# Kernel tuning notes

Measured on AMD Instinct MI355X. Metric: run time of the kernel, lower is better.

## Reference

```python
import jax, jax.numpy as jnp
import numpy as np

LN_EPS = 1e-6  # flax.linen.LayerNorm default


def setup_inputs() -> dict:
    key = jax.random.key(0)
    ks = jax.random.split(key, 16)
    N_TOT, M = 32768, 12            # total atoms, neighbors per atom
    ORIG, EDGE = 92, 41             # CGCNN atom / edge feature dims
    F, H, L = 128, 256, 3           # atom_fea_len, h_fea_len, n_conv

    def w(k, shape, fan_in):
        return jax.random.normal(k, shape, dtype=jnp.float32) / np.sqrt(fan_in).astype(np.float32)

    return {
        "atom_fea": jax.random.normal(ks[0], (N_TOT, ORIG), dtype=jnp.float32),
        "nbr_fea": jax.random.normal(ks[1], (N_TOT, M, EDGE), dtype=jnp.float32),
        "nbr_fea_idx": jax.random.randint(ks[2], (N_TOT, M), 0, N_TOT),
        # embedding Dense
        "W_embed": w(ks[3], (ORIG, F), ORIG), "b_embed": jnp.zeros((F,), jnp.float32),
        # per-conv-layer stacked params [L, ...]
        "W_center": w(ks[4], (L, F, F), F), "b_center": jnp.zeros((L, F), jnp.float32),
        "W_nbr": w(ks[5], (L, F, F), F), "b_nbr": jnp.zeros((L, F), jnp.float32),
        "W_edge": w(ks[6], (L, EDGE, F), EDGE), "b_edge": jnp.zeros((L, F), jnp.float32),
        "W_gate": w(ks[7], (L, F, F), F), "b_gate": jnp.zeros((L, F), jnp.float32),
        "W_mag": w(ks[8], (L, F, F), F), "b_mag": jnp.zeros((L, F), jnp.float32),
        "ln_scale": jnp.ones((L, F), jnp.float32), "ln_bias": jnp.zeros((L, F), jnp.float32),
        # readout: Dense(h) -> softplus -> Dense(1)
        "W_h": w(ks[9], (F, H), F), "b_h": jnp.zeros((H,), jnp.float32),
        "W_out": w(ks[10], (H, 1), H), "b_out": jnp.zeros((1,), jnp.float32),
        "batch_size": 128,
        "n_atoms_per_crystal": 256,
    }


def _layernorm(x, scale, bias):
    mu = jnp.mean(x, axis=-1, keepdims=True)
    var = jnp.mean(jnp.square(x - mu), axis=-1, keepdims=True)
    return (x - mu) * jax.lax.rsqrt(var + LN_EPS) * scale + bias


def reference(atom_fea, nbr_fea, nbr_fea_idx, W_embed, b_embed,
              W_center, b_center, W_nbr, b_nbr, W_edge, b_edge,
              W_gate, b_gate, W_mag, b_mag, ln_scale, ln_bias,
              W_h, b_h, W_out, b_out, batch_size, n_atoms_per_crystal):
    n_conv = W_center.shape[0]
    x = atom_fea @ W_embed + b_embed                       # [N, F]
    for i in range(n_conv):
        atom_nbr = jnp.take(x, nbr_fea_idx, axis=0)        # [N, M, F] gather
        # Dense on tiled center == Dense on center then broadcast
        phi_c = (x @ W_center[i] + b_center[i])[:, None, :]   # [N, 1, F]
        phi_n = atom_nbr @ W_nbr[i] + b_nbr[i]                # [N, M, F]
        phi_e = nbr_fea @ W_edge[i] + b_edge[i]               # [N, M, F]
        inter = phi_c * phi_n * phi_e                          # [N, M, F]
        gate = jax.nn.sigmoid(inter @ W_gate[i] + b_gate[i])
        mag = jax.nn.softplus(inter @ W_mag[i] + b_mag[i])
        nbr_sumed = jnp.sum(gate * mag, axis=1)               # [N, F]
        x = x + _layernorm(nbr_sumed, ln_scale[i], ln_bias[i])
    E_site = jax.nn.softplus(x @ W_h + b_h) @ W_out + b_out   # [N, 1]
    return jnp.sum(E_site.reshape(batch_size, n_atoms_per_crystal), axis=1, keepdims=True)  # [B, 1]
```

## Files before the change

kernel.cpp:

```cpp
#include <hip/hip_runtime.h>
#include <math.h>

#define N_TOT 32768
#define M_NBR 12
#define ORIG  92
#define EDGE  41
#define FD    128
#define HD    256
#define APC   256
#define NCRY  128
#define NROW  (N_TOT * M_NBR)
#define EST   48

#define WF_PER_LAYER 73728
#define WF_EMBED     12288
#define WF_H         32768

#define ISW(row, col) ((((row) << 7) + (col)) ^ (((row) & 7) << 3))

typedef __attribute__((ext_vector_type(8))) short bf16x8;
typedef __attribute__((ext_vector_type(4))) float f32x4;

union BF8 { bf16x8 v; unsigned u[4]; };

__device__ __forceinline__ unsigned pk2(float lo, float hi) {
    unsigned r;
    asm("v_cvt_pk_bf16_f32 %0, %1, %2" : "=v"(r) : "v"(lo), "v"(hi));
    return r;
}
__device__ __forceinline__ short f2bf(float f) { return (short)pk2(f, f); }
__device__ __forceinline__ float bf2f(short s) {
    union { unsigned u; float f; } v; v.u = ((unsigned)(unsigned short)s) << 16;
    return v.f;
}
__device__ __forceinline__ float softplus_f(float x) {
    return fmaxf(x, 0.0f) + 0.6931471805599453f * __log2f(1.0f + __expf(-fabsf(x)));
}
__device__ __forceinline__ float sigmoid_f(float x) {
    return __builtin_amdgcn_rcpf(1.0f + __expf(-x));
}

__global__ __launch_bounds__(256) void swizzle_kernel(
    const float* __restrict__ Wc_all, const float* __restrict__ Wn_all,
    const float* __restrict__ We_all, const float* __restrict__ Wg_all,
    const float* __restrict__ Wm_all, const float* __restrict__ W_embed,
    const float* __restrict__ W_h, const float* __restrict__ be_all,
    short* __restrict__ dst_all)
{
    int gid = blockIdx.x * 256 + threadIdx.x;
    if (gid >= 33280) return;
    const float* W; short* dst; int K_real, fid, stride, l, nt, kt;
    const float* brow = nullptr;
    if (gid < 27648) {
        int layer = gid / 9216;
        int rem = gid - layer * 9216;
        short* dbase = dst_all + layer * WF_PER_LAYER;
        if (rem < 2048)      { W = Wc_all + layer * 16384; dst = dbase;         K_real = 128; fid = rem; }
        else if (rem < 4096) { W = Wn_all + layer * 16384; dst = dbase + 16384; K_real = 128; fid = rem - 2048; }
        else if (rem < 5120) { W = We_all + layer * 5248;  dst = dbase + 32768; K_real = 41;  fid = rem - 4096;
                               brow = be_all + layer * FD; }
        else if (rem < 7168) { W = Wg_all + layer * 16384; dst = dbase + 40960; K_real = 128; fid = rem - 5120; }
        else                 { W = Wm_all + layer * 16384; dst = dbase + 57344; K_real = 128; fid = rem - 7168; }
        stride = 128; l = fid & 63; nt = (fid >> 6) & 7; kt = fid >> 9;
    } else if (gid < 29184) {
        fid = gid - 27648;
        W = W_embed; dst = dst_all + 3 * WF_PER_LAYER; K_real = ORIG; stride = 128;
        l = fid & 63; nt = (fid >> 6) & 7; kt = fid >> 9;
    } else {
        fid = gid - 29184;
        W = W_h; dst = dst_all + 3 * WF_PER_LAYER + WF_EMBED; K_real = 128; stride = 256;
        l = fid & 63; nt = (fid >> 6) & 15; kt = fid >> 10;
    }
    int n = nt * 16 + (l & 15), kb = kt * 32 + (l >> 4) * 8;
    bf16x8 v;
    #pragma unroll
    for (int j = 0; j < 8; ++j) {
        int k = kb + j;
        short val;
        if (k < K_real)                    val = f2bf(W[k * stride + n]);
        else if (brow != nullptr && k == 41) val = f2bf(brow[n]);
        else                               val = 0;
        v[j] = val;
    }
    *(bf16x8*)(dst + fid * 8) = v;
}

__global__ __launch_bounds__(256) void prep_ebf_kernel(
    const float* __restrict__ nbr_fea, short* __restrict__ ebf)
{
    const int r = blockIdx.x * 256 + threadIdx.x;
    const float* ep = nbr_fea + (long)r * EDGE;
    unsigned u[24];
    #pragma unroll
    for (int j = 0; j < 20; ++j) u[j] = pk2(ep[2 * j], ep[2 * j + 1]);
    u[20] = pk2(ep[40], 1.0f);
    u[21] = 0u; u[22] = 0u; u[23] = 0u;
    uint4* dst = (uint4*)(ebf + (long)r * EST);
    #pragma unroll
    for (int j = 0; j < 6; ++j)
        dst[j] = make_uint4(u[4 * j], u[4 * j + 1], u[4 * j + 2], u[4 * j + 3]);
}

__global__ __launch_bounds__(256) void embed_mfma_kernel(
    const float* __restrict__ atom_fea, const short* __restrict__ wef,
    const float* __restrict__ b, float* __restrict__ x, short* __restrict__ xbf)
{
    const int tid = threadIdx.x;
    const int w = tid >> 6, lane = tid & 63;
    const int q = lane >> 4, m = lane & 15;
    const int a0 = blockIdx.x * 64;
    const int arow = a0 + w * 16 + m;

    BF8 aA[3];
    const float* ap = atom_fea + (long)arow * ORIG;
    #pragma unroll
    for (int kt = 0; kt < 3; ++kt) {
        const int kb = kt * 32 + q * 8;
        BF8 t;
        if (kb + 7 < ORIG) {
            const float4 u0 = *(const float4*)(ap + kb);
            const float4 u1 = *(const float4*)(ap + kb + 4);
            t.u[0] = pk2(u0.x, u0.y); t.u[1] = pk2(u0.z, u0.w);
            t.u[2] = pk2(u1.x, u1.y); t.u[3] = pk2(u1.z, u1.w);
        } else {
            const float4 u0 = *(const float4*)(ap + kb);
            t.u[0] = pk2(u0.x, u0.y); t.u[1] = pk2(u0.z, u0.w);
            t.u[2] = 0u; t.u[3] = 0u;
        }
        aA[kt] = t;
    }

    #pragma unroll
    for (int ct = 0; ct < 8; ++ct) {
        f32x4 C = {0.f, 0.f, 0.f, 0.f};
        #pragma unroll
        for (int kt = 0; kt < 3; ++kt)
            C = __builtin_amdgcn_mfma_f32_16x16x32_bf16(
                    *(const bf16x8*)(wef + ((kt * 8 + ct) * 64 + lane) * 8), aA[kt].v, C, 0, 0, 0);
        const float4 bv = *(const float4*)(b + ct * 16 + q * 4);
        const float o0 = C[0] + bv.x, o1 = C[1] + bv.y, o2 = C[2] + bv.z, o3 = C[3] + bv.w;
        const long base = ((long)arow << 7) + ct * 16 + q * 4;
        *(float4*)(x + base) = make_float4(o0, o1, o2, o3);
        *(uint2*)(xbf + base) = make_uint2(pk2(o0, o1), pk2(o2, o3));
    }
}

__global__ __launch_bounds__(256) void pcy_kernel(
    const short* __restrict__ xbf, const short* __restrict__ wcf,
    const short* __restrict__ wnf, const float* __restrict__ bc,
    const float* __restrict__ bn, float* __restrict__ phic_g,
    float* __restrict__ y_g)
{
    const int tid = threadIdx.x;
    const int w = tid >> 6, lane = tid & 63;
    const int q = lane >> 4, m = lane & 15;
    const int arow = blockIdx.x * 64 + w * 16 + m;

    bf16x8 aX[4];
    #pragma unroll
    for (int kt = 0; kt < 4; ++kt)
        aX[kt] = *(const bf16x8*)(xbf + ((long)arow << 7) + kt * 32 + q * 8);

    #pragma unroll
    for (int ct = 0; ct < 8; ++ct) {
        f32x4 Cc = {0.f, 0.f, 0.f, 0.f};
        f32x4 Cn = {0.f, 0.f, 0.f, 0.f};
        #pragma unroll
        for (int kt = 0; kt < 4; ++kt) {
            const int fo = ((kt * 8 + ct) * 64 + lane) * 8;
            Cc = __builtin_amdgcn_mfma_f32_16x16x32_bf16(*(const bf16x8*)(wcf + fo), aX[kt], Cc, 0, 0, 0);
            Cn = __builtin_amdgcn_mfma_f32_16x16x32_bf16(*(const bf16x8*)(wnf + fo), aX[kt], Cn, 0, 0, 0);
        }
        const float4 bcv = *(const float4*)(bc + ct * 16 + q * 4);
        const float4 bnv = *(const float4*)(bn + ct * 16 + q * 4);
        const long base = ((long)arow << 7) + ct * 16 + q * 4;
        *(float4*)(phic_g + base) = make_float4(Cc[0] + bcv.x, Cc[1] + bcv.y, Cc[2] + bcv.z, Cc[3] + bcv.w);
        *(float4*)(y_g + base)    = make_float4(Cn[0] + bnv.x, Cn[1] + bnv.y, Cn[2] + bnv.z, Cn[3] + bnv.w);
    }
}

__global__ __launch_bounds__(256) void conv_mfma_kernel(
    const float* __restrict__ x_in,
    float* __restrict__ x_out, short* __restrict__ xbf_out,
    const float* __restrict__ phic_g, const float* __restrict__ y_g,
    const short* __restrict__ ebf, const int* __restrict__ nbr_idx,
    const short* __restrict__ wf,
    const float* __restrict__ bg, const float* __restrict__ bm,
    const float* __restrict__ lns, const float* __restrict__ lnb,
    const short* __restrict__ wc_next, const short* __restrict__ wn_next,
    const float* __restrict__ bc_next, const float* __restrict__ bn_next,
    float* __restrict__ phic_out, float* __restrict__ y_out)
{
    __shared__ short inter_s[192 * 128];

    const int tid = threadIdx.x;
    const int w = tid >> 6, lane = tid & 63;
    const int q = lane >> 4, m = lane & 15;
    const int a0 = blockIdx.x * 16;
    const long r0 = (long)a0 * M_NBR;

    const short* We = wf + 32768;
    const short* Wg = wf + 40960;
    const short* Wm = wf + 57344;

    int rl[3], idxv[3], atomg[3];
    #pragma unroll
    for (int i = 0; i < 3; ++i) {
        rl[i] = (w * 3 + i) * 16 + m;
        idxv[i] = nbr_idx[r0 + rl[i]];
        atomg[i] = a0 + rl[i] / 12;
    }

    bf16x8 aE[3][2];
    #pragma unroll
    for (int i = 0; i < 3; ++i) {
        const short* ep = ebf + (r0 + rl[i]) * EST;
        aE[i][0] = *(const bf16x8*)(ep + q * 8);
        if (q < 2) {
            aE[i][1] = *(const bf16x8*)(ep + 32 + q * 8);
        } else {
            BF8 z; z.u[0] = 0u; z.u[1] = 0u; z.u[2] = 0u; z.u[3] = 0u;
            aE[i][1] = z.v;
        }
    }

    #pragma unroll
    for (int ct = 0; ct < 8; ++ct) {
        f32x4 Ce[3];
        #pragma unroll
        for (int i = 0; i < 3; ++i) Ce[i] = (f32x4){0.f, 0.f, 0.f, 0.f};
        #pragma unroll
        for (int kt = 0; kt < 2; ++kt) {
            const bf16x8 efr = *(const bf16x8*)(We + ((kt * 8 + ct) * 64 + lane) * 8);
            #pragma unroll
            for (int i = 0; i < 3; ++i)
                Ce[i] = __builtin_amdgcn_mfma_f32_16x16x32_bf16(efr, aE[i][kt], Ce[i], 0, 0, 0);
        }
        #pragma unroll
        for (int i = 0; i < 3; ++i)
            *(uint2*)(inter_s + ISW(rl[i], ct * 16 + q * 4)) =
                make_uint2(pk2(Ce[i][0], Ce[i][1]), pk2(Ce[i][2], Ce[i][3]));
    }

    bf16x8 aI[3][4];
    #pragma unroll
    for (int i = 0; i < 3; ++i) {
        const float* pp = phic_g + ((long)atomg[i] << 7);
        const float* yp = y_g + ((long)idxv[i] << 7);
        #pragma unroll
        for (int kt = 0; kt < 4; ++kt) {
            const int k0 = kt * 32 + q * 8;
            const float4 pa = *(const float4*)(pp + k0);
            const float4 pb = *(const float4*)(pp + k0 + 4);
            const float4 ya = *(const float4*)(yp + k0);
            const float4 yb = *(const float4*)(yp + k0 + 4);
            const bf16x8 ef = *(const bf16x8*)(inter_s + ISW(rl[i], k0));
            const float v0 = pa.x * ya.x * bf2f(ef[0]);
            const float v1 = pa.y * ya.y * bf2f(ef[1]);
            const float v2 = pa.z * ya.z * bf2f(ef[2]);
            const float v3 = pa.w * ya.w * bf2f(ef[3]);
            const float v4 = pb.x * yb.x * bf2f(ef[4]);
            const float v5 = pb.y * yb.y * bf2f(ef[5]);
            const float v6 = pb.z * yb.z * bf2f(ef[6]);
            const float v7 = pb.w * yb.w * bf2f(ef[7]);
            BF8 t;
            t.u[0] = pk2(v0, v1); t.u[1] = pk2(v2, v3);
            t.u[2] = pk2(v4, v5); t.u[3] = pk2(v6, v7);
            aI[i][kt] = t.v;
        }
    }

    #pragma unroll
    for (int ct = 0; ct < 8; ++ct) {
        f32x4 Cg[3], Cm[3];
        #pragma unroll
        for (int i = 0; i < 3; ++i) {
            Cg[i] = (f32x4){0.f, 0.f, 0.f, 0.f};
            Cm[i] = (f32x4){0.f, 0.f, 0.f, 0.f};
        }
        #pragma unroll
        for (int kt = 0; kt < 4; ++kt) {
            const bf16x8 gfr = *(const bf16x8*)(Wg + ((kt * 8 + ct) * 64 + lane) * 8);
            const bf16x8 mfr = *(const bf16x8*)(Wm + ((kt * 8 + ct) * 64 + lane) * 8);
            #pragma unroll
            for (int i = 0; i < 3; ++i) {
                Cg[i] = __builtin_amdgcn_mfma_f32_16x16x32_bf16(gfr, aI[i][kt], Cg[i], 0, 0, 0);
                Cm[i] = __builtin_amdgcn_mfma_f32_16x16x32_bf16(mfr, aI[i][kt], Cm[i], 0, 0, 0);
            }
        }
        const float4 bgv = *(const float4*)(bg + ct * 16 + q * 4);
        const float4 bmv = *(const float4*)(bm + ct * 16 + q * 4);
        #pragma unroll
        for (int i = 0; i < 3; ++i) {
            const float v0 = sigmoid_f(Cg[i][0] + bgv.x) * softplus_f(Cm[i][0] + bmv.x);
            const float v1 = sigmoid_f(Cg[i][1] + bgv.y) * softplus_f(Cm[i][1] + bmv.y);
            const float v2 = sigmoid_f(Cg[i][2] + bgv.z) * softplus_f(Cm[i][2] + bmv.z);
            const float v3 = sigmoid_f(Cg[i][3] + bgv.w) * softplus_f(Cm[i][3] + bmv.w);
            *(uint2*)(inter_s + ISW(rl[i], ct * 16 + q * 4)) =
                make_uint2(pk2(v0, v1), pk2(v2, v3));
        }
    }

    BF8 ob;
    {
        const int a = tid >> 4;
        const int cg = tid & 15;
        float s8[8];
        #pragma unroll
        for (int j = 0; j < 8; ++j) s8[j] = 0.f;
        #pragma unroll
        for (int nb = 0; nb < 12; ++nb) {
            const bf16x8 p = *(const bf16x8*)(inter_s + ISW(a * 12 + nb, cg * 8));
            #pragma unroll
            for (int j = 0; j < 8; ++j) s8[j] += bf2f(p[j]);
        }
        float lsum = 0.f, lsq = 0.f;
        #pragma unroll
        for (int j = 0; j < 8; ++j) { lsum += s8[j]; lsq += s8[j] * s8[j]; }
        #pragma unroll
        for (int off = 1; off < 16; off <<= 1) {
            lsum += __shfl_xor(lsum, off, 64);
            lsq  += __shfl_xor(lsq,  off, 64);
        }
        const float mu = lsum * (1.0f / FD);
        float var = lsq * (1.0f / FD) - mu * mu;
        var = fmaxf(var, 0.0f);
        const float inv = rsqrtf(var + 1e-6f);
        const long xb = ((long)(a0 + a) << 7) + cg * 8;
        float xv[8], sc[4], sc2[4], bb[4], bb2[4];
        *(float4*)&xv[0] = *(const float4*)(x_in + xb);
        *(float4*)&xv[4] = *(const float4*)(x_in + xb + 4);
        *(float4*)&sc[0]  = *(const float4*)(lns + cg * 8);
        *(float4*)&sc2[0] = *(const float4*)(lns + cg * 8 + 4);
        *(float4*)&bb[0]  = *(const float4*)(lnb + cg * 8);
        *(float4*)&bb2[0] = *(const float4*)(lnb + cg * 8 + 4);
        float o[8];
        #pragma unroll
        for (int j = 0; j < 4; ++j) {
            o[j]     = xv[j]     + (s8[j]     - mu) * inv * sc[j]  + bb[j];
            o[j + 4] = xv[j + 4] + (s8[j + 4] - mu) * inv * sc2[j] + bb2[j];
        }
        ob.u[0] = pk2(o[0], o[1]); ob.u[1] = pk2(o[2], o[3]);
        ob.u[2] = pk2(o[4], o[5]); ob.u[3] = pk2(o[6], o[7]);
        *(float4*)(x_out + xb)     = make_float4(o[0], o[1], o[2], o[3]);
        *(float4*)(x_out + xb + 4) = make_float4(o[4], o[5], o[6], o[7]);
        *(bf16x8*)(xbf_out + xb)   = ob.v;
    }

    if (wc_next) {
        __syncthreads();
        *(bf16x8*)(inter_s + ISW(tid >> 4, (tid & 15) * 8)) = ob.v;
        __syncthreads();
        bf16x8 aX[4];
        #pragma unroll
        for (int kt = 0; kt < 4; ++kt)
            aX[kt] = *(const bf16x8*)(inter_s + ISW(m, kt * 32 + q * 8));
        #pragma unroll
        for (int ii = 0; ii < 2; ++ii) {
            const int ct = w * 2 + ii;
            f32x4 Cc = {0.f, 0.f, 0.f, 0.f};
            f32x4 Cn2 = {0.f, 0.f, 0.f, 0.f};
            #pragma unroll
            for (int kt = 0; kt < 4; ++kt) {
                const int fo = ((kt * 8 + ct) * 64 + lane) * 8;
                Cc  = __builtin_amdgcn_mfma_f32_16x16x32_bf16(*(const bf16x8*)(wc_next + fo), aX[kt], Cc, 0, 0, 0);
                Cn2 = __builtin_amdgcn_mfma_f32_16x16x32_bf16(*(const bf16x8*)(wn_next + fo), aX[kt], Cn2, 0, 0, 0);
            }
            const float4 bcv = *(const float4*)(bc_next + ct * 16 + q * 4);
            const float4 bnv = *(const float4*)(bn_next + ct * 16 + q * 4);
            const long base = ((long)(a0 + m) << 7) + ct * 16 + q * 4;
            *(float4*)(phic_out + base) =
                make_float4(Cc[0] + bcv.x, Cc[1] + bcv.y, Cc[2] + bcv.z, Cc[3] + bcv.w);
            *(float4*)(y_out + base) =
                make_float4(Cn2[0] + bnv.x, Cn2[1] + bnv.y, Cn2[2] + bnv.z, Cn2[3] + bnv.w);
        }
    }
}

__global__ __launch_bounds__(256) void readout_mfma_kernel(
    const short* __restrict__ xbf, const short* __restrict__ whf,
    const float* __restrict__ bh, const float* __restrict__ Wo,
    const float* __restrict__ bo, float* __restrict__ out)
{
    const int tid = threadIdx.x;
    const int w = tid >> 6, lane = tid & 63;
    const int q = lane >> 4, m = lane & 15;
    const int a0 = blockIdx.x * 64;
    const int arow = a0 + w * 16 + m;

    bf16x8 aX[4];
    #pragma unroll
    for (int kt = 0; kt < 4; ++kt)
        aX[kt] = *(const bf16x8*)(xbf + ((long)arow << 7) + kt * 32 + q * 8);

    float e[4] = {0.f, 0.f, 0.f, 0.f};
    #pragma unroll
    for (int nt = 0; nt < 16; ++nt) {
        f32x4 C = {0.f, 0.f, 0.f, 0.f};
        #pragma unroll
        for (int kt = 0; kt < 4; ++kt)
            C = __builtin_amdgcn_mfma_f32_16x16x32_bf16(
                    aX[kt], *(const bf16x8*)(whf + ((kt * 16 + nt) * 64 + lane) * 8), C, 0, 0, 0);
        const int col = nt * 16 + m;
        const float bhv = bh[col], wov = Wo[col];
        #pragma unroll
        for (int r = 0; r < 4; ++r)
            e[r] += softplus_f(C[r] + bhv) * wov;
    }
    float esum = e[0] + e[1] + e[2] + e[3];
    #pragma unroll
    for (int off = 32; off > 0; off >>= 1)
        esum += __shfl_xor(esum, off, 64);
    if (lane == 0)
        atomicAdd(&out[a0 / APC], esum + 16.0f * bo[0]);
}

__global__ void zero_out_kernel(float* __restrict__ out) {
    if (threadIdx.x < NCRY) out[threadIdx.x] = 0.0f;
}

extern "C" void kernel_launch(void* const* d_in, const int* in_sizes, int n_in,
                              void* d_out, int out_size, void* d_ws, size_t ws_size,
                              hipStream_t stream) {
    const float* atom_fea = (const float*)d_in[0];
    const float* nbr_fea  = (const float*)d_in[1];
    const int*   nbr_idx  = (const int*)d_in[2];
    const float* W_embed  = (const float*)d_in[3];
    const float* b_embed  = (const float*)d_in[4];
    const float* W_center = (const float*)d_in[5];
    const float* b_center = (const float*)d_in[6];
    const float* W_nbr    = (const float*)d_in[7];
    const float* b_nbr    = (const float*)d_in[8];
    const float* W_edge   = (const float*)d_in[9];
    const float* b_edge   = (const float*)d_in[10];
    const float* W_gate   = (const float*)d_in[11];
    const float* b_gate   = (const float*)d_in[12];
    const float* W_mag    = (const float*)d_in[13];
    const float* b_mag    = (const float*)d_in[14];
    const float* ln_scale = (const float*)d_in[15];
    const float* ln_bias  = (const float*)d_in[16];
    const float* W_h      = (const float*)d_in[17];
    const float* b_h      = (const float*)d_in[18];
    const float* W_out    = (const float*)d_in[19];
    const float* b_out    = (const float*)d_in[20];

    float* out = (float*)d_out;
    const size_t NX = (size_t)N_TOT * FD;
    float* xA    = (float*)d_ws;
    float* xB    = xA + NX;
    float* phic  = xB + NX;
    float* yA    = phic + NX;
    float* yB    = yA + NX;
    short* xbfA  = (short*)(yB + NX);
    short* xbfB  = xbfA + NX;
    short* ebf   = xbfB + NX;
    short* wfrag = ebf + (size_t)NROW * EST;

    swizzle_kernel<<<130, 256, 0, stream>>>(W_center, W_nbr, W_edge, W_gate, W_mag,
                                            W_embed, W_h, b_edge, wfrag);
    prep_ebf_kernel<<<NROW / 256, 256, 0, stream>>>(nbr_fea, ebf);
    embed_mfma_kernel<<<N_TOT / 64, 256, 0, stream>>>(
        atom_fea, wfrag + 3 * WF_PER_LAYER, b_embed, xA, xbfA);
    pcy_kernel<<<N_TOT / 64, 256, 0, stream>>>(
        xbfA, wfrag, wfrag + 16384, b_center, b_nbr, phic, yA);

    conv_mfma_kernel<<<N_TOT / 16, 256, 0, stream>>>(
        xA, xB, xbfB, phic, yA, ebf, nbr_idx, wfrag,
        b_gate, b_mag, ln_scale, ln_bias,
        wfrag + WF_PER_LAYER, wfrag + WF_PER_LAYER + 16384,
        b_center + FD, b_nbr + FD, phic, yB);
    conv_mfma_kernel<<<N_TOT / 16, 256, 0, stream>>>(
        xB, xA, xbfA, phic, yB, ebf, nbr_idx, wfrag + WF_PER_LAYER,
        b_gate + FD, b_mag + FD, ln_scale + FD, ln_bias + FD,
        wfrag + 2 * WF_PER_LAYER, wfrag + 2 * WF_PER_LAYER + 16384,
        b_center + 2 * FD, b_nbr + 2 * FD, phic, yA);
    conv_mfma_kernel<<<N_TOT / 16, 256, 0, stream>>>(
        xA, xB, xbfB, phic, yA, ebf, nbr_idx, wfrag + 2 * WF_PER_LAYER,
        b_gate + 2 * FD, b_mag + 2 * FD, ln_scale + 2 * FD, ln_bias + 2 * FD,
        nullptr, nullptr, nullptr, nullptr, nullptr, nullptr);

    zero_out_kernel<<<1, 128, 0, stream>>>(out);
    readout_mfma_kernel<<<N_TOT / 64, 256, 0, stream>>>(
        xbfB, wfrag + 3 * WF_PER_LAYER + WF_EMBED, b_h, W_out, b_out, out);
}
```

Measured before the change: 436.2 us.

## Fuse edge prep, embedding and first-layer projections into one front kernel

```diff
diff --git a/kernel.cpp b/kernel.cpp
--- a/kernel.cpp
+++ b/kernel.cpp
@@ -11,6 +11,8 @@
 #define NCRY  128
 #define NROW  (N_TOT * M_NBR)
 #define EST   48
+#define NBLK_EMBED (N_TOT / 64)
+#define NBLK_PREP  (NROW / 256)
 
 #define WF_PER_LAYER 73728
 #define WF_EMBED     12288
@@ -77,39 +79,46 @@
     for (int j = 0; j < 8; ++j) {
         int k = kb + j;
         short val;
-        if (k < K_real)                    val = f2bf(W[k * stride + n]);
+        if (k < K_real)                      val = f2bf(W[k * stride + n]);
         else if (brow != nullptr && k == 41) val = f2bf(brow[n]);
-        else                               val = 0;
+        else                                 val = 0;
         v[j] = val;
     }
     *(bf16x8*)(dst + fid * 8) = v;
 }
 
-__global__ __launch_bounds__(256) void prep_ebf_kernel(
+__global__ __launch_bounds__(256) void front_kernel(
+    const float* __restrict__ atom_fea, const short* __restrict__ wef,
+    const float* __restrict__ b, float* __restrict__ x, short* __restrict__ xbf,
+    const short* __restrict__ wcf, const short* __restrict__ wnf,
+    const float* __restrict__ bc, const float* __restrict__ bn,
+    float* __restrict__ phic_g, float* __restrict__ y_g,
     const float* __restrict__ nbr_fea, short* __restrict__ ebf)
 {
-    const int r = blockIdx.x * 256 + threadIdx.x;
-    const float* ep = nbr_fea + (long)r * EDGE;
-    unsigned u[24];
-    #pragma unroll
-    for (int j = 0; j < 20; ++j) u[j] = pk2(ep[2 * j], ep[2 * j + 1]);
-    u[20] = pk2(ep[40], 1.0f);
-    u[21] = 0u; u[22] = 0u; u[23] = 0u;
-    uint4* dst = (uint4*)(ebf + (long)r * EST);
-    #pragma unroll
-    for (int j = 0; j < 6; ++j)
-        dst[j] = make_uint4(u[4 * j], u[4 * j + 1], u[4 * j + 2], u[4 * j + 3]);
-}
-
-__global__ __launch_bounds__(256) void embed_mfma_kernel(
-    const float* __restrict__ atom_fea, const short* __restrict__ wef,
-    const float* __restrict__ b, float* __restrict__ x, short* __restrict__ xbf)
-{
+    __shared__ short xs_s[4 * 16 * 128];
+
     const int tid = threadIdx.x;
+
+    if (blockIdx.x >= NBLK_EMBED) {
+        const int r = (blockIdx.x - NBLK_EMBED) * 256 + tid;
+        const float* ep = nbr_fea + (long)r * EDGE;
+        unsigned u[24];
+        #pragma unroll
+        for (int j = 0; j < 20; ++j) u[j] = pk2(ep[2 * j], ep[2 * j + 1]);
+        u[20] = pk2(ep[40], 1.0f);
+        u[21] = 0u; u[22] = 0u; u[23] = 0u;
+        uint4* dst = (uint4*)(ebf + (long)r * EST);
+        #pragma unroll
+        for (int j = 0; j < 6; ++j)
+            dst[j] = make_uint4(u[4 * j], u[4 * j + 1], u[4 * j + 2], u[4 * j + 3]);
+        return;
+    }
+
     const int w = tid >> 6, lane = tid & 63;
     const int q = lane >> 4, m = lane & 15;
     const int a0 = blockIdx.x * 64;
     const int arow = a0 + w * 16 + m;
+    short* xs = xs_s + w * 2048;
 
     BF8 aA[3];
     const float* ap = atom_fea + (long)arow * ORIG;
@@ -140,27 +149,16 @@
         const float4 bv = *(const float4*)(b + ct * 16 + q * 4);
         const float o0 = C[0] + bv.x, o1 = C[1] + bv.y, o2 = C[2] + bv.z, o3 = C[3] + bv.w;
         const long base = ((long)arow << 7) + ct * 16 + q * 4;
+        const uint2 ou = make_uint2(pk2(o0, o1), pk2(o2, o3));
         *(float4*)(x + base) = make_float4(o0, o1, o2, o3);
-        *(uint2*)(xbf + base) = make_uint2(pk2(o0, o1), pk2(o2, o3));
-    }
-}
-
-__global__ __launch_bounds__(256) void pcy_kernel(
-    const short* __restrict__ xbf, const short* __restrict__ wcf,
-    const short* __restrict__ wnf, const float* __restrict__ bc,
-    const float* __restrict__ bn, float* __restrict__ phic_g,
-    float* __restrict__ y_g)
-{
-    const int tid = threadIdx.x;
-    const int w = tid >> 6, lane = tid & 63;
-    const int q = lane >> 4, m = lane & 15;
-    const int arow = blockIdx.x * 64 + w * 16 + m;
+        *(uint2*)(xbf + base) = ou;
+        *(uint2*)(xs + ISW(m, ct * 16 + q * 4)) = ou;
+    }
 
     bf16x8 aX[4];
     #pragma unroll
     for (int kt = 0; kt < 4; ++kt)
-        aX[kt] = *(const bf16x8*)(xbf + ((long)arow << 7) + kt * 32 + q * 8);
-
+        aX[kt] = *(const bf16x8*)(xs + ISW(m, kt * 32 + q * 8));
     #pragma unroll
     for (int ct = 0; ct < 8; ++ct) {
         f32x4 Cc = {0.f, 0.f, 0.f, 0.f};
@@ -458,11 +456,10 @@
 
     swizzle_kernel<<<130, 256, 0, stream>>>(W_center, W_nbr, W_edge, W_gate, W_mag,
                                             W_embed, W_h, b_edge, wfrag);
-    prep_ebf_kernel<<<NROW / 256, 256, 0, stream>>>(nbr_fea, ebf);
-    embed_mfma_kernel<<<N_TOT / 64, 256, 0, stream>>>(
-        atom_fea, wfrag + 3 * WF_PER_LAYER, b_embed, xA, xbfA);
-    pcy_kernel<<<N_TOT / 64, 256, 0, stream>>>(
-        xbfA, wfrag, wfrag + 16384, b_center, b_nbr, phic, yA);
+    front_kernel<<<NBLK_EMBED + NBLK_PREP, 256, 0, stream>>>(
+        atom_fea, wfrag + 3 * WF_PER_LAYER, b_embed, xA, xbfA,
+        wfrag, wfrag + 16384, b_center, b_nbr, phic, yA,
+        nbr_fea, ebf);
 
     conv_mfma_kernel<<<N_TOT / 16, 256, 0, stream>>>(
         xA, xB, xbfB, phic, yA, ebf, nbr_idx, wfrag,
```

Result: no change. 436.8 us (+0.1%).
